# Kernel optimization log

Measured on AMD Instinct MI355X. Metric: run time of the kernel, lower is better.

Reference implementation:

```python
import jax, jax.numpy as jnp
import numpy as np

N_NODES = 100000
N_EDGES = 600000
D = 128


def setup_inputs() -> dict:
    key = jax.random.key(0)
    k1, k2, k3, k4, k5, k6 = jax.random.split(key, 6)
    feat = jax.random.normal(k1, (N_NODES, D), dtype=jnp.float32)
    src = jax.random.randint(k2, (N_EDGES,), 0, N_NODES, dtype=jnp.int64)
    dst = jax.random.randint(k3, (N_EDGES,), 0, N_NODES, dtype=jnp.int64)
    W_neigh = jax.random.normal(k4, (D, D), dtype=jnp.float32) * (1.0 / np.sqrt(D))
    b_neigh = jax.random.normal(k5, (D,), dtype=jnp.float32) * 0.02
    W_self = jax.random.normal(k6, (D, D), dtype=jnp.float32) * (1.0 / np.sqrt(D))
    return {"feat": feat, "src": src, "dst": dst,
            "W_neigh": W_neigh, "b_neigh": b_neigh, "W_self": W_self}


def reference(feat, src, dst, W_neigh, b_neigh, W_self):
    # DGL GraphConv(norm='none'): sum-aggregate neighbor features, then linear.
    # agg[i] = sum_{(s->i) in E} feat[s]
    agg = jax.ops.segment_sum(feat[src], dst, num_segments=feat.shape[0])  # [N, D]
    neigh_feat = agg @ W_neigh + b_neigh                                   # [N, Dout]
    self_feat = feat @ W_self                                              # [N, Dout]
    return neigh_feat + self_feat
```

## Files before the change

kernel.cpp:

```cpp
#include <hip/hip_runtime.h>

#define DF 128
#define KX 256
#define CAP 16
#define GR 64
#define PBLK 1024

typedef __attribute__((ext_vector_type(8))) short short8;
typedef __attribute__((ext_vector_type(4))) float v4f;

__device__ __forceinline__ unsigned short f2bf(float x) {
    unsigned u = __float_as_uint(x);
    unsigned r = (u + 0x7FFFu + ((u >> 16) & 1u)) >> 16;
    return (unsigned short)r;
}
__device__ __forceinline__ float bf2f(unsigned short h) {
    return __uint_as_float((unsigned)h << 16);
}
__device__ __forceinline__ unsigned pack2(float a, float b) {
    return (unsigned)f2bf(a) | ((unsigned)f2bf(b) << 16);
}

__global__ __launch_bounds__(256) void prep_kernel(
    const int* __restrict__ idx32, int nE, int* __restrict__ hdr,
    const float* __restrict__ Wn, const float* __restrict__ Ws,
    unsigned short* __restrict__ Bt2, int* __restrict__ counts, int cnt_ints,
    const float* __restrict__ feat, unsigned short* __restrict__ Fbf,
    int M, int nzb)
{
    const int b = blockIdx.x;
    const int t = threadIdx.x;
    if (b == 0) {
        __shared__ int sh;
        if (t == 0) sh = 0;
        __syncthreads();
        int found = 0;
        for (int i = t; i < 2048 && i < nE; i += 256)
            if (idx32[2 * i + 1] != 0) found = 1;
        if (found) sh = 1;
        __syncthreads();
        if (t == 0) { hdr[0] = sh; hdr[1] = 0; }
        if (t < 64)
            reinterpret_cast<unsigned*>(Fbf + (size_t)M * DF)[t] = 0u;
    } else if (b <= 128) {
        int idx = (b - 1) * 256 + t;
        int n = idx >> 8, k = idx & 255;
        float v = (k < DF) ? Wn[(size_t)k * DF + n]
                           : Ws[(size_t)(k - DF) * DF + n];
        Bt2[idx] = f2bf(v);
    } else if (b <= 128 + nzb) {
        int off = ((b - 129) * 256 + t) * 4;
        if (off < cnt_ints)
            *reinterpret_cast<int4*>(counts + off) = make_int4(0, 0, 0, 0);
    } else {
        const long long base = ((long long)(b - 129 - nzb) * 2048 + t * 8);
        const long long total = (long long)M * DF;
        if (base + 8 <= total) {
            float4 v0 = *reinterpret_cast<const float4*>(feat + base);
            float4 v1 = *reinterpret_cast<const float4*>(feat + base + 4);
            uint4 pk;
            pk.x = pack2(v0.x, v0.y);
            pk.y = pack2(v0.z, v0.w);
            pk.z = pack2(v1.x, v1.y);
            pk.w = pack2(v1.z, v1.w);
            *reinterpret_cast<uint4*>(Fbf + base) = pk;
        }
    }
}

__global__ __launch_bounds__(256) void place_kernel(
    const void* __restrict__ src, const void* __restrict__ dst, int nE,
    int* __restrict__ hdr, int* __restrict__ counts, int* __restrict__ buckets,
    int2* __restrict__ ovf)
{
    const int t = threadIdx.x;
    const int is32 = hdr[0];
    const int stride = PBLK * 256;
    if (is32) {
        const int* sp = (const int*)src;
        const int* dp = (const int*)dst;
        for (int e = blockIdx.x * 256 + t; e < nE; e += stride) {
            int s = sp[e], d = dp[e];
            int pos = atomicAdd(&counts[d], 1);
            if (pos < CAP) {
                buckets[(size_t)d * CAP + pos] = s;
            } else {
                int oi = atomicAdd(&hdr[1], 1);
                ovf[oi] = make_int2(s, d);
            }
        }
    } else {
        const long long* sp = (const long long*)src;
        const long long* dp = (const long long*)dst;
        for (int e = blockIdx.x * 256 + t; e < nE; e += stride) {
            int s = (int)sp[e], d = (int)dp[e];
            int pos = atomicAdd(&counts[d], 1);
            if (pos < CAP) {
                buckets[(size_t)d * CAP + pos] = s;
            } else {
                int oi = atomicAdd(&hdr[1], 1);
                ovf[oi] = make_int2(s, d);
            }
        }
    }
}

__global__ __launch_bounds__(256) void agg_gemm_kernel(
    const unsigned short* __restrict__ Fbf, const unsigned short* __restrict__ Bt2,
    const float* __restrict__ bias, float* __restrict__ out, int M,
    const int* __restrict__ counts, const int* __restrict__ buckets,
    const int* __restrict__ hdr, const int2* __restrict__ ovf)
{
    __shared__ unsigned short As[GR][KX + 8];

    const int t = threadIdx.x;
    const int block_row = blockIdx.x * GR;

    const int wave = t >> 6;
    const int lane = t & 63;
    const int nl   = lane & 15;
    const int quad = lane >> 4;

    const int n0 = wave * 32;
    short8 bfrag[2][8];
#pragma unroll
    for (int ct = 0; ct < 2; ct++)
#pragma unroll
        for (int kk = 0; kk < 8; kk++)
            bfrag[ct][kk] = *reinterpret_cast<const short8*>(
                Bt2 + (size_t)(n0 + ct * 16 + nl) * KX + kk * 32 + quad * 8);
    float bcol[2];
#pragma unroll
    for (int ct = 0; ct < 2; ct++)
        bcol[ct] = bias[n0 + ct * 16 + nl];

    {
        const int gi = t >> 4;
        const int li = t & 15;
        const size_t lo = (size_t)li * 8;
        const int n_ovf = hdr[1];

#define LDF(s) (*reinterpret_cast<const uint4*>(Fbf + (size_t)(s) * DF + lo))
#define ACC8(Y) do { \
        a0 += bf2f((unsigned short)((Y).x)); a1 += bf2f((unsigned short)((Y).x >> 16)); \
        a2 += bf2f((unsigned short)((Y).y)); a3 += bf2f((unsigned short)((Y).y >> 16)); \
        a4 += bf2f((unsigned short)((Y).z)); a5 += bf2f((unsigned short)((Y).z >> 16)); \
        a6 += bf2f((unsigned short)((Y).w)); a7 += bf2f((unsigned short)((Y).w >> 16)); \
    } while (0)

#pragma unroll
        for (int j = 0; j < 4; j++) {
            const int r_local = gi * 4 + j;
            const int grow = block_row + r_local;
            const int deg_raw = (grow < M) ? counts[grow] : 0;
            const int deg = min(deg_raw, CAP);
            const int* b = buckets + (size_t)((grow < M) ? grow : 0) * CAP;

            float a0 = 0.f, a1 = 0.f, a2 = 0.f, a3 = 0.f;
            float a4 = 0.f, a5 = 0.f, a6 = 0.f, a7 = 0.f;

            int4 sa = *reinterpret_cast<const int4*>(b);
            int4 sb = *reinterpret_cast<const int4*>(b + 4);
            const int i0 = (0 < deg) ? sa.x : M;
            const int i1 = (1 < deg) ? sa.y : M;
            const int i2 = (2 < deg) ? sa.z : M;
            const int i3 = (3 < deg) ? sa.w : M;
            const int i4 = (4 < deg) ? sb.x : M;
            const int i5 = (5 < deg) ? sb.y : M;
            const int i6 = (6 < deg) ? sb.z : M;
            const int i7 = (7 < deg) ? sb.w : M;
            uint4 y0 = LDF(i0);
            uint4 y1 = LDF(i1);
            uint4 y2 = LDF(i2);
            uint4 y3 = LDF(i3);
            uint4 y4 = LDF(i4);
            uint4 y5 = LDF(i5);
            uint4 y6 = LDF(i6);
            uint4 y7 = LDF(i7);
            uint4 sf = LDF((grow < M) ? grow : M);
            ACC8(y0); ACC8(y1); ACC8(y2); ACC8(y3);
            ACC8(y4); ACC8(y5); ACC8(y6); ACC8(y7);

            if (deg > 8) {
                int4 sc = *reinterpret_cast<const int4*>(b + 8);
                int4 sd = *reinterpret_cast<const int4*>(b + 12);
                const int j0 = ( 8 < deg) ? sc.x : M;
                const int j1 = ( 9 < deg) ? sc.y : M;
                const int j2 = (10 < deg) ? sc.z : M;
                const int j3 = (11 < deg) ? sc.w : M;
                const int j4 = (12 < deg) ? sd.x : M;
                const int j5 = (13 < deg) ? sd.y : M;
                const int j6 = (14 < deg) ? sd.z : M;
                const int j7 = (15 < deg) ? sd.w : M;
                uint4 z0 = LDF(j0);
                uint4 z1 = LDF(j1);
                uint4 z2 = LDF(j2);
                uint4 z3 = LDF(j3);
                uint4 z4 = LDF(j4);
                uint4 z5 = LDF(j5);
                uint4 z6 = LDF(j6);
                uint4 z7 = LDF(j7);
                ACC8(z0); ACC8(z1); ACC8(z2); ACC8(z3);
                ACC8(z4); ACC8(z5); ACC8(z6); ACC8(z7);
            }

            if (deg_raw > CAP) {
                for (int i = 0; i < n_ovf; i++) {
                    int2 sd2 = ovf[i];
                    if (sd2.y == grow) {
                        uint4 y = LDF(sd2.x);
                        ACC8(y);
                    }
                }
            }

            uint4 pk;
            pk.x = pack2(a0, a1);
            pk.y = pack2(a2, a3);
            pk.z = pack2(a4, a5);
            pk.w = pack2(a6, a7);
            *reinterpret_cast<uint4*>(&As[r_local][lo])      = pk;
            *reinterpret_cast<uint4*>(&As[r_local][DF + lo]) = sf;
        }
#undef LDF
#undef ACC8
    }

    __syncthreads();

#pragma unroll
    for (int rt = 0; rt < 4; rt++) {
        short8 afrag[8];
#pragma unroll
        for (int kk = 0; kk < 8; kk++)
            afrag[kk] = *reinterpret_cast<const short8*>(
                &As[rt * 16 + nl][kk * 32 + quad * 8]);
#pragma unroll
        for (int ct = 0; ct < 2; ct++) {
            v4f acc = {0.f, 0.f, 0.f, 0.f};
#pragma unroll
            for (int kk = 0; kk < 8; kk++)
                acc = __builtin_amdgcn_mfma_f32_16x16x32_bf16(
                    afrag[kk], bfrag[ct][kk], acc, 0, 0, 0);
            const int n = n0 + ct * 16 + nl;
            const int lrow = rt * 16 + quad * 4;
#pragma unroll
            for (int r = 0; r < 4; r++) {
                const int grow = block_row + lrow + r;
                if (grow < M)
                    out[(size_t)grow * DF + n] = acc[r] + bcol[ct];
            }
        }
    }
}

extern "C" void kernel_launch(void* const* d_in, const int* in_sizes, int n_in,
                              void* d_out, int out_size, void* d_ws, size_t ws_size,
                              hipStream_t stream) {
    const float* feat = (const float*)d_in[0];
    const void*  src  = d_in[1];
    const void*  dst  = d_in[2];
    const float* Wn   = (const float*)d_in[3];
    const float* bias = (const float*)d_in[4];
    const float* Wsf  = (const float*)d_in[5];
    float* out = (float*)d_out;

    const int M  = in_sizes[0] / DF;
    const int nE = in_sizes[1];

    const size_t cnt_off   = 256;
    const size_t cnt_bytes = (((size_t)(M + 64) * 4) + 255) & ~(size_t)255;
    const size_t bkt_off   = cnt_off + cnt_bytes;
    const size_t bkt_bytes = (size_t)M * CAP * sizeof(int);
    const size_t bt_off    = (bkt_off + bkt_bytes + 255) & ~(size_t)255;
    const size_t bt_bytes  = (size_t)DF * KX * sizeof(unsigned short);
    const size_t f_off     = bt_off + bt_bytes;
    const size_t f_bytes   = (size_t)(M + 1) * DF * sizeof(unsigned short);
    const size_t ovf_off   = (f_off + f_bytes + 255) & ~(size_t)255;

    int*            hdr     = (int*)d_ws;
    int*            counts  = (int*)((char*)d_ws + cnt_off);
    int*            buckets = (int*)((char*)d_ws + bkt_off);
    unsigned short* Bt2     = (unsigned short*)((char*)d_ws + bt_off);
    unsigned short* Fbf     = (unsigned short*)((char*)d_ws + f_off);
    int2*           ovf     = (int2*)((char*)d_ws + ovf_off);

    const int cnt_ints = (int)(cnt_bytes / 4);
    const int nzb = (cnt_ints + 1023) / 1024;
    const long long total = (long long)M * DF;
    const int nconv = (int)((total + 2047) / 2048);

    prep_kernel<<<1 + 128 + nzb + nconv, 256, 0, stream>>>(
        (const int*)src, nE, hdr, Wn, Wsf, Bt2, counts, cnt_ints,
        feat, Fbf, M, nzb);

    place_kernel<<<PBLK, 256, 0, stream>>>(
        src, dst, nE, hdr, counts, buckets, ovf);

    const int gemm_blocks = (M + GR - 1) / GR;
    agg_gemm_kernel<<<gemm_blocks, 256, 0, stream>>>(
        Fbf, Bt2, bias, out, M, counts, buckets, hdr, ovf);
}
```

Measured before the change: 199.1 us.

## Fuse edge placement into prep kernel, memset counters, swizzle shared A tile

```diff
diff --git a/kernel.cpp b/kernel.cpp
--- a/kernel.cpp
+++ b/kernel.cpp
@@ -4,7 +4,6 @@
 #define KX 256
 #define CAP 16
 #define GR 64
-#define PBLK 1024
 
 typedef __attribute__((ext_vector_type(8))) short short8;
 typedef __attribute__((ext_vector_type(4))) float v4f;
@@ -21,41 +20,54 @@
     return (unsigned)f2bf(a) | ((unsigned)f2bf(b) << 16);
 }
 
-__global__ __launch_bounds__(256) void prep_kernel(
-    const int* __restrict__ idx32, int nE, int* __restrict__ hdr,
+__global__ __launch_bounds__(256) void mega_kernel(
+    const void* __restrict__ src, const void* __restrict__ dst, int nE,
+    int* __restrict__ hdr, int* __restrict__ counts, int* __restrict__ buckets,
+    int2* __restrict__ ovf,
     const float* __restrict__ Wn, const float* __restrict__ Ws,
-    unsigned short* __restrict__ Bt2, int* __restrict__ counts, int cnt_ints,
+    unsigned short* __restrict__ Bt2,
     const float* __restrict__ feat, unsigned short* __restrict__ Fbf,
-    int M, int nzb)
+    int M, int NPB)
 {
     const int b = blockIdx.x;
     const int t = threadIdx.x;
-    if (b == 0) {
-        __shared__ int sh;
-        if (t == 0) sh = 0;
-        __syncthreads();
-        int found = 0;
-        for (int i = t; i < 2048 && i < nE; i += 256)
-            if (idx32[2 * i + 1] != 0) found = 1;
-        if (found) sh = 1;
-        __syncthreads();
-        if (t == 0) { hdr[0] = sh; hdr[1] = 0; }
-        if (t < 64)
-            reinterpret_cast<unsigned*>(Fbf + (size_t)M * DF)[t] = 0u;
-    } else if (b <= 128) {
-        int idx = (b - 1) * 256 + t;
+
+    if (b < NPB) {
+        const int* p32 = (const int*)src;
+        const int lane = t & 63;
+        const int sbase = (t >> 6) * 64 + lane;
+        const int pred = (p32[2 * sbase + 1] | p32[2 * (sbase + 256) + 1]) != 0;
+        const bool is32 = (__ballot(pred) != 0ull);
+
+        const int e = b * 256 + t;
+        if (e < nE) {
+            int s, d;
+            if (is32) {
+                s = ((const int*)src)[e];
+                d = ((const int*)dst)[e];
+            } else {
+                s = (int)((const long long*)src)[e];
+                d = (int)((const long long*)dst)[e];
+            }
+            int pos = atomicAdd(&counts[d], 1);
+            if (pos < CAP) {
+                buckets[(size_t)d * CAP + pos] = s;
+            } else {
+                int oi = atomicAdd(&hdr[1], 1);
+                ovf[oi] = make_int2(s, d);
+            }
+        }
+    } else if (b < NPB + 128) {
+        int idx = (b - NPB) * 256 + t;
         int n = idx >> 8, k = idx & 255;
         float v = (k < DF) ? Wn[(size_t)k * DF + n]
                            : Ws[(size_t)(k - DF) * DF + n];
         Bt2[idx] = f2bf(v);
-    } else if (b <= 128 + nzb) {
-        int off = ((b - 129) * 256 + t) * 4;
-        if (off < cnt_ints)
-            *reinterpret_cast<int4*>(counts + off) = make_int4(0, 0, 0, 0);
     } else {
-        const long long base = ((long long)(b - 129 - nzb) * 2048 + t * 8);
-        const long long total = (long long)M * DF;
-        if (base + 8 <= total) {
+        const long long base = ((long long)(b - NPB - 128) * 2048 + t * 8);
+        const long long mtot = (long long)M * DF;
+        const long long ttot = (long long)(M + 1) * DF;
+        if (base + 8 <= mtot) {
             float4 v0 = *reinterpret_cast<const float4*>(feat + base);
             float4 v1 = *reinterpret_cast<const float4*>(feat + base + 4);
             uint4 pk;
@@ -64,46 +76,13 @@
             pk.z = pack2(v1.x, v1.y);
             pk.w = pack2(v1.z, v1.w);
             *reinterpret_cast<uint4*>(Fbf + base) = pk;
+        } else if (base + 8 <= ttot) {
+            *reinterpret_cast<uint4*>(Fbf + base) = make_uint4(0u, 0u, 0u, 0u);
         }
     }
 }
 
-__global__ __launch_bounds__(256) void place_kernel(
-    const void* __restrict__ src, const void* __restrict__ dst, int nE,
-    int* __restrict__ hdr, int* __restrict__ counts, int* __restrict__ buckets,
-    int2* __restrict__ ovf)
-{
-    const int t = threadIdx.x;
-    const int is32 = hdr[0];
-    const int stride = PBLK * 256;
-    if (is32) {
-        const int* sp = (const int*)src;
-        const int* dp = (const int*)dst;
-        for (int e = blockIdx.x * 256 + t; e < nE; e += stride) {
-            int s = sp[e], d = dp[e];
-            int pos = atomicAdd(&counts[d], 1);
-            if (pos < CAP) {
-                buckets[(size_t)d * CAP + pos] = s;
-            } else {
-                int oi = atomicAdd(&hdr[1], 1);
-                ovf[oi] = make_int2(s, d);
-            }
-        }
-    } else {
-        const long long* sp = (const long long*)src;
-        const long long* dp = (const long long*)dst;
-        for (int e = blockIdx.x * 256 + t; e < nE; e += stride) {
-            int s = (int)sp[e], d = (int)dp[e];
-            int pos = atomicAdd(&counts[d], 1);
-            if (pos < CAP) {
-                buckets[(size_t)d * CAP + pos] = s;
-            } else {
-                int oi = atomicAdd(&hdr[1], 1);
-                ovf[oi] = make_int2(s, d);
-            }
-        }
-    }
-}
+#define ASW(r, u) (((r) << 5) + ((u) ^ ((r) & 7)))
 
 __global__ __launch_bounds__(256) void agg_gemm_kernel(
     const unsigned short* __restrict__ Fbf, const unsigned short* __restrict__ Bt2,
@@ -111,7 +90,7 @@
     const int* __restrict__ counts, const int* __restrict__ buckets,
     const int* __restrict__ hdr, const int2* __restrict__ ovf)
 {
-    __shared__ unsigned short As[GR][KX + 8];
+    __shared__ uint4 As16[GR * 32];
 
     const int t = threadIdx.x;
     const int block_row = blockIdx.x * GR;
@@ -219,8 +198,8 @@
             pk.y = pack2(a2, a3);
             pk.z = pack2(a4, a5);
             pk.w = pack2(a6, a7);
-            *reinterpret_cast<uint4*>(&As[r_local][lo])      = pk;
-            *reinterpret_cast<uint4*>(&As[r_local][DF + lo]) = sf;
+            As16[ASW(r_local, li)]      = pk;
+            As16[ASW(r_local, 16 + li)] = sf;
         }
 #undef LDF
 #undef ACC8
@@ -230,11 +209,12 @@
 
 #pragma unroll
     for (int rt = 0; rt < 4; rt++) {
+        const int arow = rt * 16 + nl;
         short8 afrag[8];
 #pragma unroll
         for (int kk = 0; kk < 8; kk++)
             afrag[kk] = *reinterpret_cast<const short8*>(
-                &As[rt * 16 + nl][kk * 32 + quad * 8]);
+                &As16[ASW(arow, kk * 4 + quad)]);
 #pragma unroll
         for (int ct = 0; ct < 2; ct++) {
             v4f acc = {0.f, 0.f, 0.f, 0.f};
@@ -285,17 +265,15 @@
     unsigned short* Fbf     = (unsigned short*)((char*)d_ws + f_off);
     int2*           ovf     = (int2*)((char*)d_ws + ovf_off);
 
-    const int cnt_ints = (int)(cnt_bytes / 4);
-    const int nzb = (cnt_ints + 1023) / 1024;
-    const long long total = (long long)M * DF;
-    const int nconv = (int)((total + 2047) / 2048);
-
-    prep_kernel<<<1 + 128 + nzb + nconv, 256, 0, stream>>>(
-        (const int*)src, nE, hdr, Wn, Wsf, Bt2, counts, cnt_ints,
-        feat, Fbf, M, nzb);
-
-    place_kernel<<<PBLK, 256, 0, stream>>>(
-        src, dst, nE, hdr, counts, buckets, ovf);
+    hipMemsetAsync(d_ws, 0, cnt_off + cnt_bytes, stream);
+
+    const int NPB = (nE + 255) / 256;
+    const long long ttot = (long long)(M + 1) * DF;
+    const int nconv = (int)((ttot + 2047) / 2048);
+
+    mega_kernel<<<NPB + 128 + nconv, 256, 0, stream>>>(
+        src, dst, nE, hdr, counts, buckets, ovf,
+        Wn, Wsf, Bt2, feat, Fbf, M, NPB);
 
     const int gemm_blocks = (M + GR - 1) / GR;
     agg_gemm_kernel<<<gemm_blocks, 256, 0, stream>>>(
```

New measurement: 188.2 us. 1.06x faster.
